# Kernel tuning notes

Hardware: AMD Instinct MI355X
Metric: run time of the kernel (lower is better)

Reference implementation:

```python
import jax, jax.numpy as jnp
import numpy as np

H, W, PART = 16, 16, 4
EPS = 1e-5


def _window_rows(h, part):
    # Static, boundary-clamped window row indices, as in position_aware_max.
    pr = h // part
    half = pr // 2
    idx = []
    for i in range(h):
        u, l = i - half, i + half
        if u < 0:
            u, l = 0, pr
        if l > h:
            u, l = h - pr, h
        idx.append(np.arange(u, l))
    return np.stack(idx)  # [h, pr] (uniform length since pr is even)


def _pam(s6, row_idx, dim):
    # s6: [p, g, hr, wr, hc, wc]; row index r = hr*W + wr, col index s = hc*W + wc.
    if dim == 0:
        # per column block i (hc == i): max over rows hr in window, all wr; keep wc
        sc = jnp.moveaxis(s6, 4, 0)  # [hc, p, g, hr, wr, wc]
        f = lambda sci, idx: jnp.take(sci, idx, axis=2).max(axis=(2, 3))
    else:
        # per row block i (hr == i): max over cols hc in window, all wc; keep wr
        sc = jnp.moveaxis(s6, 2, 0)  # [hr, p, g, wr, hc, wc]
        f = lambda sci, idx: jnp.take(sci, idx, axis=3).max(axis=(3, 4))
    out = jax.vmap(f)(sc, jnp.asarray(row_idx))  # [h, p, g, w]
    p, g = s6.shape[0], s6.shape[1]
    return jnp.transpose(out, (1, 2, 0, 3)).reshape(p, g, -1)  # [p, g, hw]


def _bn(x, gamma, beta, axes):
    # BatchNorm in training mode: biased batch statistics (torch default).
    m = x.mean(axis=axes, keepdims=True)
    v = x.var(axis=axes, keepdims=True)
    return gamma * (x - m) * jax.lax.rsqrt(v + EPS) + beta


def setup_inputs() -> dict:
    key = jax.random.key(0)
    k0, k1, k2 = jax.random.split(key, 3)
    p, g, c = 48, 48, 64
    hw = H * W
    return {
        "prob_fea": jax.random.normal(k0, (p, c, H, W), jnp.float32),
        "gal_fea": jax.random.normal(k1, (g, c, H, W), jnp.float32),
        "bn_gamma": jnp.ones((1,), jnp.float32),
        "bn_beta": jnp.zeros((1,), jnp.float32),
        "fc_w": jnp.full((1, hw), 1.0 / hw, jnp.float32),  # reset_parameters fill
        "fc_b": jax.random.normal(k2, (1,), jnp.float32) * 0.01,
        "lbn_gamma": jnp.ones((1,), jnp.float32),
        "lbn_beta": jnp.zeros((1,), jnp.float32),
    }


def reference(prob_fea, gal_fea, bn_gamma, bn_beta, fc_w, fc_b, lbn_gamma, lbn_beta):
    p, c = prob_fea.shape[0], prob_fea.shape[1]
    g = gal_fea.shape[0]
    hw = H * W
    pf = prob_fea.reshape(p, c, hw)
    gf = gal_fea.reshape(g, c, hw)
    score = jnp.einsum('pcs,gcr->pgrs', pf, gf)  # [p, g, hw, hw]
    s6 = score.reshape(p, g, H, W, H, W)
    row_idx = _window_rows(H, PART)
    s1 = _pam(s6, row_idx, 0)  # [p, g, hw]
    s2 = _pam(s6, row_idx, 1)  # [p, g, hw]
    sc = jnp.concatenate([s1, s2], axis=-1).reshape(-1, 1, hw)  # [2*p*g, 1, hw]
    sc = _bn(sc, bn_gamma, bn_beta, (0, 2)).reshape(-1, hw)
    sc = sc @ fc_w.T + fc_b  # [2*p*g, 1]
    sc = sc.reshape(-1, 2).sum(axis=1, keepdims=True)  # [p*g, 1]
    sc = _bn(sc, lbn_gamma, lbn_beta, (0,))
    return jax.nn.sigmoid(sc).reshape(p, g)
```

## Files before the change

kernel.cpp:

```cpp
#include <hip/hip_runtime.h>

typedef __attribute__((ext_vector_type(8))) short short8;
typedef __attribute__((ext_vector_type(4))) float float4v;

__constant__ int LOW[24] = {0,0,0,1,2,3,4,5,6,7,8,9,10,11,12,12,
                            99,99,99,99,99,99,99,99};
__constant__ int HIW[24] = {3,3,3,4,5,6,7,8,9,10,11,12,13,14,15,15,
                            -1,-1,-1,-1,-1,-1,-1,-1};
__constant__ int CTLO[4] = {0, 2, 6, 10};

__device__ __forceinline__ unsigned short f2bf(float f) {
    unsigned int x = __builtin_bit_cast(unsigned int, f);
    x += 0x7FFF + ((x >> 16) & 1);
    return (unsigned short)(x >> 16);
}

struct __align__(16) U16x8 { unsigned short u[8]; };

template <int CTRL>
__device__ __forceinline__ float dppmaxf(float x) {
    int y = __builtin_amdgcn_update_dpp(0, __builtin_bit_cast(int, x),
                                        CTRL, 0xF, 0xF, true);
    return fmaxf(x, __builtin_bit_cast(float, y));
}
__device__ __forceinline__ float rowmax16(float x) {
    x = dppmaxf<0xB1>(x);
    x = dppmaxf<0x4E>(x);
    x = dppmaxf<0x141>(x);
    x = dppmaxf<0x140>(x);
    return x;
}

__global__ __launch_bounds__(256) void pretranspose_kernel(
    const float* __restrict__ prob,
    const float* __restrict__ gal,
    unsigned short* __restrict__ outT)
{
    const int img = blockIdx.x;
    const float* src = (img < 48) ? (prob + img * 16384)
                                  : (gal + (img - 48) * 16384);
    unsigned short* dst = outT + img * 16384;
    const int tid = threadIdx.x;
    const int c0 = (tid & 7) * 8;
    const int s0 = (tid >> 3) * 8;
    unsigned short v[8][8];
#pragma unroll
    for (int i = 0; i < 8; ++i) {
        const float* p = src + (c0 + i) * 256 + s0;
        const float4v f0 = *(const float4v*)(p);
        const float4v f1 = *(const float4v*)(p + 4);
        v[i][0] = f2bf(f0.x); v[i][1] = f2bf(f0.y);
        v[i][2] = f2bf(f0.z); v[i][3] = f2bf(f0.w);
        v[i][4] = f2bf(f1.x); v[i][5] = f2bf(f1.y);
        v[i][6] = f2bf(f1.z); v[i][7] = f2bf(f1.w);
    }
#pragma unroll
    for (int j = 0; j < 8; ++j) {
        U16x8 o;
#pragma unroll
        for (int i = 0; i < 8; ++i) o.u[i] = v[i][j];
        const int srow = s0 + j;
        const int off = srow * 64 + (((c0 >> 3) ^ (srow & 7)) << 3);
        *(U16x8*)(dst + off) = o;
    }
}

__global__ __launch_bounds__(256, 4) void score_pam_kernel(
    const unsigned short* __restrict__ preT,
    const float* __restrict__ fcw,
    float* __restrict__ outDot,
    float* __restrict__ outSum,
    float* __restrict__ outSq)
{
    __shared__ float s1part[4][8][4][16];
    __shared__ float redA[4][4][4];
    __shared__ float redB[4][4];

    const int tid = threadIdx.x;
    const int pair = blockIdx.x;
    const int ip = pair / 48;
    const int ig = pair % 48;
    const unsigned short* pimg = preT + ip * 16384;
    const unsigned short* gimg = preT + (48 + ig) * 16384;

    const int lane = tid & 63;
    const int w = tid >> 6;
    const int laneM = lane & 15;
    const int q = lane >> 4;
    const int z = laneM & 7;

    const int rtb = 4 * w;
    int lo2[4], hi2[4];
#pragma unroll
    for (int j = 0; j < 4; ++j) { lo2[j] = LOW[rtb + j]; hi2[j] = HIW[rtb + j]; }
    const int ctbase = CTLO[w];

    short8 a0[4], a1[4];
#pragma unroll
    for (int j = 0; j < 4; ++j) {
        const int srow = (rtb + j) * 16 + laneM;
        a0[j] = *(const short8*)(gimg + srow * 64 + ((q ^ z) << 3));
        a1[j] = *(const short8*)(gimg + srow * 64 + (((q + 4) ^ z) << 3));
    }

    float4v run[4];
#pragma unroll
    for (int j = 0; j < 4; ++j)
        run[j] = (float4v){ -3.0e38f, -3.0e38f, -3.0e38f, -3.0e38f };
    float s1p[8];
#pragma unroll
    for (int i = 0; i < 8; ++i) s1p[i] = -3.0e38f;

#pragma unroll
    for (int i = 0; i < 8; ++i) {
        const int ctr = ctbase + i;
        const int ctc = (ctr > 15) ? 15 : ctr;
        const int sl = ctc * 16 + laneM;
        const short8 b0 = *(const short8*)(pimg + sl * 64 + ((q ^ z) << 3));
        const short8 b1 = *(const short8*)(pimg + sl * 64 + (((q + 4) ^ z) << 3));
        const int wl = LOW[ctr], wh = HIW[ctr];
#pragma unroll
        for (int j = 0; j < 4; ++j) {
            const int rt = rtb + j;
            const bool c2 = (ctr >= lo2[j]) && (ctr <= hi2[j]);
            const bool c1 = (rt >= wl) && (rt <= wh);
            if (c1 || c2) {
                float4v acc = { 0.f, 0.f, 0.f, 0.f };
                acc = __builtin_amdgcn_mfma_f32_16x16x32_bf16(a0[j], b0, acc, 0, 0, 0);
                acc = __builtin_amdgcn_mfma_f32_16x16x32_bf16(a1[j], b1, acc, 0, 0, 0);
                if (c2) {
                    run[j].x = fmaxf(run[j].x, acc.x);
                    run[j].y = fmaxf(run[j].y, acc.y);
                    run[j].z = fmaxf(run[j].z, acc.z);
                    run[j].w = fmaxf(run[j].w, acc.w);
                }
                if (c1) {
                    const float t = fmaxf(fmaxf(acc.x, acc.y), fmaxf(acc.z, acc.w));
                    s1p[i] = fmaxf(s1p[i], t);
                }
            }
        }
    }

    float dot = 0.f, sum = 0.f, sq = 0.f;
    const float msk = (laneM == 0) ? 1.0f : 0.0f;
#pragma unroll
    for (int j = 0; j < 4; ++j) {
        const float rx = rowmax16(run[j].x);
        const float ry = rowmax16(run[j].y);
        const float rz = rowmax16(run[j].z);
        const float rw = rowmax16(run[j].w);
        const float4v fw = *(const float4v*)(fcw + (rtb + j) * 16 + q * 4);
        float t;
        t = msk * rx; dot += t * fw.x; sum += t; sq += t * rx;
        t = msk * ry; dot += t * fw.y; sum += t; sq += t * ry;
        t = msk * rz; dot += t * fw.z; sum += t; sq += t * rz;
        t = msk * rw; dot += t * fw.w; sum += t; sq += t * rw;
    }
    if (laneM == 0) { redA[w][q][0] = dot; redA[w][q][1] = sum; redA[w][q][2] = sq; }

#pragma unroll
    for (int i = 0; i < 8; ++i) s1part[w][i][q][laneM] = s1p[i];
    __syncthreads();

    {
        const int hc = tid >> 4;
        const int col = tid & 15;
        float v = -3.0e38f;
#pragma unroll
        for (int wv = 0; wv < 4; ++wv) {
            const int ii = hc - CTLO[wv];
            if (ii >= 0 && ii < 8) {
#pragma unroll
                for (int q2 = 0; q2 < 4; ++q2)
                    v = fmaxf(v, s1part[wv][ii][q2][col]);
            }
        }
        float d1 = v * fcw[tid];
        float s1v = v;
        float q1 = v * v;
#pragma unroll
        for (int d = 32; d >= 1; d >>= 1) {
            d1 += __shfl_down(d1, d, 64);
            s1v += __shfl_down(s1v, d, 64);
            q1 += __shfl_down(q1, d, 64);
        }
        if (lane == 0) { redB[w][0] = d1; redB[w][1] = s1v; redB[w][2] = q1; }
    }
    __syncthreads();

    if (tid < 3) {
        float s = 0.f;
#pragma unroll
        for (int a = 0; a < 4; ++a) {
#pragma unroll
            for (int b = 0; b < 4; ++b) s += redA[a][b][tid];
            s += redB[a][tid];
        }
        if (tid == 0) outDot[pair] = s;
        else if (tid == 1) outSum[pair] = s;
        else outSq[pair] = s;
    }
}

__global__ __launch_bounds__(256) void finalize_kernel(
    const float* __restrict__ dDot,
    const float* __restrict__ dSum,
    const float* __restrict__ dSq,
    const float* __restrict__ bng,
    const float* __restrict__ bnb,
    const float* __restrict__ fcw,
    const float* __restrict__ fcb,
    const float* __restrict__ lg,
    const float* __restrict__ lb,
    float* __restrict__ outp)
{
    __shared__ float red[12];
    const int tid = threadIdx.x;
    const int lane = tid & 63;
    const int w = tid >> 6;

    float S = 0.f, Q = 0.f;
    float dv[9];
#pragma unroll
    for (int k = 0; k < 9; ++k) {
        const int i = tid + 256 * k;
        dv[k] = dDot[i];
        S += dSum[i];
        Q += dSq[i];
    }
    float Wj = fcw[tid];
#pragma unroll
    for (int d = 32; d >= 1; d >>= 1) {
        S += __shfl_down(S, d, 64);
        Q += __shfl_down(Q, d, 64);
        Wj += __shfl_down(Wj, d, 64);
    }
    if (lane == 0) { red[w] = S; red[4 + w] = Q; red[8 + w] = Wj; }
    __syncthreads();
    S = red[0] + red[1] + red[2] + red[3];
    Q = red[4] + red[5] + red[6] + red[7];
    const float W = red[8] + red[9] + red[10] + red[11];
    __syncthreads();

    const float N1 = 1179648.0f;
    const float m1 = S / N1;
    const float v1 = Q / N1 - m1 * m1;
    const float inv1 = rsqrtf(v1 + 1e-5f);
    const float g1 = bng[0], b1 = bnb[0], fb = fcb[0];
    const float g2 = lg[0], b2 = lb[0];
    const float cA = g1 * inv1;
    const float cB = 2.f * (b1 * W + fb) - cA * 2.f * m1 * W;

    float Sy = 0.f, Qy = 0.f;
    float yv[9];
#pragma unroll
    for (int k = 0; k < 9; ++k) {
        const float y = cA * dv[k] + cB;
        yv[k] = y;
        Sy += y;
        Qy += y * y;
    }
#pragma unroll
    for (int d = 32; d >= 1; d >>= 1) {
        Sy += __shfl_down(Sy, d, 64);
        Qy += __shfl_down(Qy, d, 64);
    }
    if (lane == 0) { red[w] = Sy; red[4 + w] = Qy; }
    __syncthreads();
    Sy = red[0] + red[1] + red[2] + red[3];
    Qy = red[4] + red[5] + red[6] + red[7];

    const float m2 = Sy / 2304.0f;
    const float v2 = Qy / 2304.0f - m2 * m2;
    const float inv2 = rsqrtf(v2 + 1e-5f);
#pragma unroll
    for (int k = 0; k < 9; ++k) {
        const int i = tid + 256 * k;
        const float z = g2 * (yv[k] - m2) * inv2 + b2;
        outp[i] = 1.0f / (1.0f + __expf(-z));
    }
}

extern "C" void kernel_launch(void* const* d_in, const int* in_sizes, int n_in,
                              void* d_out, int out_size, void* d_ws, size_t ws_size,
                              hipStream_t stream) {
    const float* prob = (const float*)d_in[0];
    const float* gal  = (const float*)d_in[1];
    const float* bng  = (const float*)d_in[2];
    const float* bnb  = (const float*)d_in[3];
    const float* fcw  = (const float*)d_in[4];
    const float* fcb  = (const float*)d_in[5];
    const float* lg   = (const float*)d_in[6];
    const float* lb   = (const float*)d_in[7];

    unsigned short* preT = (unsigned short*)d_ws;
    float* ws = (float*)((char*)d_ws + 96 * 16384 * sizeof(unsigned short));
    float* dDot = ws;
    float* dSum = ws + 2304;
    float* dSq  = ws + 4608;

    hipLaunchKernelGGL(pretranspose_kernel, dim3(96), dim3(256), 0, stream,
                       prob, gal, preT);
    hipLaunchKernelGGL(score_pam_kernel, dim3(48 * 48), dim3(256), 0, stream,
                       preT, fcw, dDot, dSum, dSq);
    hipLaunchKernelGGL(finalize_kernel, dim3(1), dim3(256), 0, stream,
                       dDot, dSum, dSq, bng, bnb, fcw, fcb, lg, lb,
                       (float*)d_out);
}
```

Measured before the change: 97.91 us.

## Replace block reductions with DPP row sums and global atomics; preload B fragments

Per-pair dot/sum/square partials are no longer gathered through shared memory with a final __syncthreads. Instead each 16-lane row reduces with DPP and lane 0 issues atomicAdds straight to global, and the pretranspose kernel zeroes the accumulators. All eight B fragments are loaded up front so the MFMA loop has no load latency inside it, and the occupancy hint drops from 4 to 3 blocks per CU to leave room for the extra registers. The cost is many more global atomics per block (12 per wave plus 3 per 16 threads), float atomic ordering that is not deterministic, and possibly lower occupancy.

```diff
diff --git a/kernel.cpp b/kernel.cpp
--- a/kernel.cpp
+++ b/kernel.cpp
@@ -22,6 +22,12 @@
     int y = __builtin_amdgcn_update_dpp(0, __builtin_bit_cast(int, x),
                                         CTRL, 0xF, 0xF, true);
     return fmaxf(x, __builtin_bit_cast(float, y));
+}
+template <int CTRL>
+__device__ __forceinline__ float dppaddf(float x) {
+    int y = __builtin_amdgcn_update_dpp(0, __builtin_bit_cast(int, x),
+                                        CTRL, 0xF, 0xF, true);
+    return x + __builtin_bit_cast(float, y);
 }
 __device__ __forceinline__ float rowmax16(float x) {
     x = dppmaxf<0xB1>(x);
@@ -30,12 +36,23 @@
     x = dppmaxf<0x140>(x);
     return x;
 }
+__device__ __forceinline__ float rowsum16(float x) {
+    x = dppaddf<0xB1>(x);
+    x = dppaddf<0x4E>(x);
+    x = dppaddf<0x141>(x);
+    x = dppaddf<0x140>(x);
+    return x;
+}
 
 __global__ __launch_bounds__(256) void pretranspose_kernel(
     const float* __restrict__ prob,
     const float* __restrict__ gal,
-    unsigned short* __restrict__ outT)
+    unsigned short* __restrict__ outT,
+    float* __restrict__ accums)
 {
+    const int gidx = blockIdx.x * 256 + threadIdx.x;
+    if (gidx < 6912) accums[gidx] = 0.0f;
+
     const int img = blockIdx.x;
     const float* src = (img < 48) ? (prob + img * 16384)
                                   : (gal + (img - 48) * 16384);
@@ -65,7 +82,7 @@
     }
 }
 
-__global__ __launch_bounds__(256, 4) void score_pam_kernel(
+__global__ __launch_bounds__(256, 3) void score_pam_kernel(
     const unsigned short* __restrict__ preT,
     const float* __restrict__ fcw,
     float* __restrict__ outDot,
@@ -73,8 +90,6 @@
     float* __restrict__ outSq)
 {
     __shared__ float s1part[4][8][4][16];
-    __shared__ float redA[4][4][4];
-    __shared__ float redB[4][4];
 
     const int tid = threadIdx.x;
     const int pair = blockIdx.x;
@@ -102,22 +117,27 @@
         a0[j] = *(const short8*)(gimg + srow * 64 + ((q ^ z) << 3));
         a1[j] = *(const short8*)(gimg + srow * 64 + (((q + 4) ^ z) << 3));
     }
-
-    float4v run[4];
-#pragma unroll
-    for (int j = 0; j < 4; ++j)
-        run[j] = (float4v){ -3.0e38f, -3.0e38f, -3.0e38f, -3.0e38f };
-    float s1p[8];
-#pragma unroll
-    for (int i = 0; i < 8; ++i) s1p[i] = -3.0e38f;
-
+    short8 B0[8], B1[8];
 #pragma unroll
     for (int i = 0; i < 8; ++i) {
         const int ctr = ctbase + i;
         const int ctc = (ctr > 15) ? 15 : ctr;
         const int sl = ctc * 16 + laneM;
-        const short8 b0 = *(const short8*)(pimg + sl * 64 + ((q ^ z) << 3));
-        const short8 b1 = *(const short8*)(pimg + sl * 64 + (((q + 4) ^ z) << 3));
+        B0[i] = *(const short8*)(pimg + sl * 64 + ((q ^ z) << 3));
+        B1[i] = *(const short8*)(pimg + sl * 64 + (((q + 4) ^ z) << 3));
+    }
+
+    float4v run[4];
+#pragma unroll
+    for (int j = 0; j < 4; ++j)
+        run[j] = (float4v){ -3.0e38f, -3.0e38f, -3.0e38f, -3.0e38f };
+    float s1p[8];
+#pragma unroll
+    for (int i = 0; i < 8; ++i) s1p[i] = -3.0e38f;
+
+#pragma unroll
+    for (int i = 0; i < 8; ++i) {
+        const int ctr = ctbase + i;
         const int wl = LOW[ctr], wh = HIW[ctr];
 #pragma unroll
         for (int j = 0; j < 4; ++j) {
@@ -126,8 +146,8 @@
             const bool c1 = (rt >= wl) && (rt <= wh);
             if (c1 || c2) {
                 float4v acc = { 0.f, 0.f, 0.f, 0.f };
-                acc = __builtin_amdgcn_mfma_f32_16x16x32_bf16(a0[j], b0, acc, 0, 0, 0);
-                acc = __builtin_amdgcn_mfma_f32_16x16x32_bf16(a1[j], b1, acc, 0, 0, 0);
+                acc = __builtin_amdgcn_mfma_f32_16x16x32_bf16(a0[j], B0[i], acc, 0, 0, 0);
+                acc = __builtin_amdgcn_mfma_f32_16x16x32_bf16(a1[j], B1[i], acc, 0, 0, 0);
                 if (c2) {
                     run[j].x = fmaxf(run[j].x, acc.x);
                     run[j].y = fmaxf(run[j].y, acc.y);
@@ -142,22 +162,25 @@
         }
     }
 
-    float dot = 0.f, sum = 0.f, sq = 0.f;
-    const float msk = (laneM == 0) ? 1.0f : 0.0f;
-#pragma unroll
-    for (int j = 0; j < 4; ++j) {
-        const float rx = rowmax16(run[j].x);
-        const float ry = rowmax16(run[j].y);
-        const float rz = rowmax16(run[j].z);
-        const float rw = rowmax16(run[j].w);
-        const float4v fw = *(const float4v*)(fcw + (rtb + j) * 16 + q * 4);
-        float t;
-        t = msk * rx; dot += t * fw.x; sum += t; sq += t * rx;
-        t = msk * ry; dot += t * fw.y; sum += t; sq += t * ry;
-        t = msk * rz; dot += t * fw.z; sum += t; sq += t * rz;
-        t = msk * rw; dot += t * fw.w; sum += t; sq += t * rw;
-    }
-    if (laneM == 0) { redA[w][q][0] = dot; redA[w][q][1] = sum; redA[w][q][2] = sq; }
+    {
+        float dot = 0.f, sum = 0.f, sq = 0.f;
+#pragma unroll
+        for (int j = 0; j < 4; ++j) {
+            const float rx = rowmax16(run[j].x);
+            const float ry = rowmax16(run[j].y);
+            const float rz = rowmax16(run[j].z);
+            const float rw = rowmax16(run[j].w);
+            const float4v fw = *(const float4v*)(fcw + (rtb + j) * 16 + q * 4);
+            dot += rx * fw.x + ry * fw.y + rz * fw.z + rw * fw.w;
+            sum += rx + ry + rz + rw;
+            sq  += rx * rx + ry * ry + rz * rz + rw * rw;
+        }
+        if (laneM == 0) {
+            atomicAdd(&outDot[pair], dot);
+            atomicAdd(&outSum[pair], sum);
+            atomicAdd(&outSq[pair], sq);
+        }
+    }
 
 #pragma unroll
     for (int i = 0; i < 8; ++i) s1part[w][i][q][laneM] = s1p[i];
@@ -176,30 +199,14 @@
                     v = fmaxf(v, s1part[wv][ii][q2][col]);
             }
         }
-        float d1 = v * fcw[tid];
-        float s1v = v;
-        float q1 = v * v;
-#pragma unroll
-        for (int d = 32; d >= 1; d >>= 1) {
-            d1 += __shfl_down(d1, d, 64);
-            s1v += __shfl_down(s1v, d, 64);
-            q1 += __shfl_down(q1, d, 64);
-        }
-        if (lane == 0) { redB[w][0] = d1; redB[w][1] = s1v; redB[w][2] = q1; }
-    }
-    __syncthreads();
-
-    if (tid < 3) {
-        float s = 0.f;
-#pragma unroll
-        for (int a = 0; a < 4; ++a) {
-#pragma unroll
-            for (int b = 0; b < 4; ++b) s += redA[a][b][tid];
-            s += redB[a][tid];
-        }
-        if (tid == 0) outDot[pair] = s;
-        else if (tid == 1) outSum[pair] = s;
-        else outSq[pair] = s;
+        float d1 = rowsum16(v * fcw[tid]);
+        float s1v = rowsum16(v);
+        float q1 = rowsum16(v * v);
+        if (laneM == 0) {
+            atomicAdd(&outDot[pair], d1);
+            atomicAdd(&outSum[pair], s1v);
+            atomicAdd(&outSq[pair], q1);
+        }
     }
 }
 
@@ -301,7 +308,7 @@
     float* dSq  = ws + 4608;
 
     hipLaunchKernelGGL(pretranspose_kernel, dim3(96), dim3(256), 0, stream,
-                       prob, gal, preT);
+                       prob, gal, preT, dDot);
     hipLaunchKernelGGL(score_pam_kernel, dim3(48 * 48), dim3(256), 0, stream,
                        preT, fcw, dDot, dSum, dSq);
     hipLaunchKernelGGL(finalize_kernel, dim3(1), dim3(256), 0, stream,
```

Result: slower. 108.0 us (+10.3%).
